# Kernel tuning notes

Hardware: AMD Instinct MI355X
Metric: run time of the kernel (lower is better)

## Reference

```python
import jax, jax.numpy as jnp
import numpy as np

N_NODES = 40000
N_EDGES = 400000
N_GRAPHS = 256
F_IN = 128
COND = 100
HEADS = 32
DIMS = [90, 45, 15, 5]
EPS = 1e-5


def setup_inputs() -> dict:
    key = jax.random.key(0)
    ks = iter(jax.random.split(key, 64))
    inp = {}
    inp["x"] = jax.random.normal(next(ks), (N_NODES, F_IN), dtype=jnp.float32)
    inp["edge_index"] = jax.random.randint(next(ks), (2, N_EDGES), 0, N_NODES, dtype=jnp.int32)
    inp["batch"] = jnp.sort(jax.random.randint(next(ks), (N_NODES,), 0, N_GRAPHS, dtype=jnp.int32))
    inp["conditional_features"] = jax.random.normal(next(ks), (COND,), dtype=jnp.float32)
    # GATConv params: W [in, H*C], a_src/a_dst [H, C], bias [C] (concat=False -> out is C)
    dims_in = [F_IN] + DIMS[:-1]
    for i, (ci, co) in enumerate(zip(dims_in, DIMS), start=1):
        sw = 1.0 / np.sqrt(ci)
        inp[f"W{i}"] = jax.random.normal(next(ks), (ci, HEADS * co), dtype=jnp.float32) * sw
        inp[f"as{i}"] = jax.random.normal(next(ks), (HEADS, co), dtype=jnp.float32) * (1.0 / np.sqrt(co))
        inp[f"ad{i}"] = jax.random.normal(next(ks), (HEADS, co), dtype=jnp.float32) * (1.0 / np.sqrt(co))
        inp[f"b{i}"] = jnp.zeros((co,), dtype=jnp.float32)
    # BatchNorm affine params (init gamma=1, beta=0) for sizes F_IN,90,45,15,5
    for i, c in enumerate([F_IN] + DIMS, start=1):
        inp[f"g{i}"] = jnp.ones((c,), dtype=jnp.float32)
        inp[f"be{i}"] = jnp.zeros((c,), dtype=jnp.float32)
    inp["fcW"] = jax.random.normal(next(ks), (DIMS[-1] + COND, 1), dtype=jnp.float32) * (1.0 / np.sqrt(DIMS[-1] + COND))
    inp["fcb"] = jnp.zeros((1,), dtype=jnp.float32)
    return inp


def _bn(x, g, b):
    # training-mode BatchNorm1d: batch statistics (biased var), eps=1e-5
    mu = x.mean(0)
    var = x.var(0)
    return g * (x - mu) * jax.lax.rsqrt(var + EPS) + b


def _gat(x, W, a_s, a_d, b, src, dst, n):
    H, C = a_s.shape
    h = (x @ W).reshape(n, H, C)                      # [N,H,C]
    s_src = jnp.einsum("nhc,hc->nh", h, a_s)
    s_dst = jnp.einsum("nhc,hc->nh", h, a_d)
    logit = jax.nn.leaky_relu(s_src[src] + s_dst[dst], 0.2)  # [E,H]
    m = jax.ops.segment_max(logit, dst, num_segments=n)
    e = jnp.exp(logit - m[dst])
    denom = jax.ops.segment_sum(e, dst, num_segments=n)
    alpha = e / denom[dst]                            # per-dst softmax, [E,H]
    out = jnp.zeros((n, C), dtype=x.dtype)
    for hi in range(H):  # fixed small loop over heads keeps peak memory at [E,C]
        out = out + jax.ops.segment_sum(alpha[:, hi, None] * h[src, hi, :], dst, num_segments=n)
    return out / H + b   # concat=False -> mean over heads, then bias


def reference(x, edge_index, batch, conditional_features,
              W1, as1, ad1, b1, W2, as2, ad2, b2, W3, as3, ad3, b3, W4, as4, ad4, b4,
              g1, be1, g2, be2, g3, be3, g4, be4, g5, be5, fcW, fcb):
    n = x.shape[0]
    loop = jnp.arange(n, dtype=edge_index.dtype)      # PyG GATConv adds self-loops by default
    src = jnp.concatenate([edge_index[0], loop])
    dst = jnp.concatenate([edge_index[1], loop])

    h = _bn(x, g1, be1)
    h = jax.nn.leaky_relu(_gat(h, W1, as1, ad1, b1, src, dst, n), 0.01)
    h = _bn(h, g2, be2)
    h = jax.nn.leaky_relu(_gat(h, W2, as2, ad2, b2, src, dst, n), 0.01)
    h = _bn(h, g3, be3)
    h = jax.nn.leaky_relu(_gat(h, W3, as3, ad3, b3, src, dst, n), 0.01)
    h = _bn(h, g4, be4)
    h = jax.nn.leaky_relu(_gat(h, W4, as4, ad4, b4, src, dst, n), 0.01)
    # dropout is identity in eval mode

    counts = jax.ops.segment_sum(jnp.ones((n,), dtype=h.dtype), batch, num_segments=N_GRAPHS)
    pooled = jax.ops.segment_sum(h, batch, num_segments=N_GRAPHS) / jnp.maximum(counts, 1.0)[:, None]
    z = jnp.concatenate([pooled, jnp.broadcast_to(conditional_features, (N_GRAPHS, COND))], axis=1)
    return jax.nn.sigmoid(z @ fcW + fcb).reshape(-1, 1)
```

## Files before the change

kernel.cpp:

```cpp
#include <hip/hip_runtime.h>
#include <hip/hip_bf16.h>

constexpr int NN = 40000;
constexpr int NE = 400000;
constexpr int NSLAB = 20000;
constexpr int MPAD = 20096;
constexpr int MPADX = 40192;
constexpr int SCB = 256;
constexpr int SCHUNK = (NN + SCB - 1) / SCB;
constexpr int NPB = 512;

__device__ __forceinline__ unsigned short f2bf(float f) {
    unsigned int u = __float_as_uint(f);
    unsigned int r = (u + 0x7FFFu + ((u >> 16) & 1u)) >> 16;
    return (unsigned short)r;
}

__device__ __forceinline__ unsigned int cvt_pk_bf16(float a, float b) {
    unsigned int r;
    asm("v_cvt_pk_bf16_f32 %0, %1, %2" : "=v"(r) : "v"(a), "v"(b));
    return r;
}

__device__ __forceinline__ void load_lds16(const unsigned short* g, unsigned short* l) {
    __builtin_amdgcn_global_load_lds(
        (const __attribute__((address_space(1))) unsigned int*)(g),
        (__attribute__((address_space(3))) unsigned int*)(l), 16, 0, 0);
}

typedef __attribute__((ext_vector_type(8))) short bf16x8;
typedef __attribute__((ext_vector_type(4))) float f32x4;

__global__ void bn_partial(const float* __restrict__ x, int N, int C,
                           float* __restrict__ partial) {
    int ch = threadIdx.x;
    if (ch >= C) return;
    float s = 0.f, sq = 0.f;
    for (int n = blockIdx.x; n < N; n += gridDim.x) {
        float v = x[(size_t)n * C + ch];
        s += v; sq += v * v;
    }
    partial[(size_t)blockIdx.x * 2 * C + ch]     = s;
    partial[(size_t)blockIdx.x * 2 * C + C + ch] = sq;
}

template <int CIN, int CP, int NB>
__global__ __launch_bounds__(256) void bn_apply_f(const float* __restrict__ x,
                                                  const float* __restrict__ partial,
                                                  const float* __restrict__ g,
                                                  const float* __restrict__ be,
                                                  float* __restrict__ scale_g,
                                                  float* __restrict__ shift_g,
                                                  unsigned short* __restrict__ xbn) {
    __shared__ float hs[2][128], hq[2][128];
    __shared__ float sc_l[CP], sh_l[CP];
    const int tid = threadIdx.x;
    const int half = tid >> 7, ch = tid & 127;
    if (ch < CIN) {
        constexpr int H = NB / 2;
        int b0 = half ? H : 0;
        int b1 = half ? NB : H;
        float s = 0.f, sq = 0.f;
#pragma unroll 8
        for (int b = b0; b < b1; ++b) {
            s  += partial[(size_t)b * 2 * CIN + ch];
            sq += partial[(size_t)b * 2 * CIN + CIN + ch];
        }
        hs[half][ch] = s; hq[half][ch] = sq;
    }
    __syncthreads();
    if (tid < CP) {
        float sc = 0.f, sh = 0.f;
        if (tid < CIN) {
            float s  = hs[0][tid] + hs[1][tid];
            float sq = hq[0][tid] + hq[1][tid];
            float mean = s / (float)NN;
            float var  = sq / (float)NN - mean * mean;
            float inv  = rsqrtf(var + 1e-5f);
            sc = g[tid] * inv;
            sh = be[tid] - mean * sc;
            if (blockIdx.x == 0) { scale_g[tid] = sc; shift_g[tid] = sh; }
        }
        sc_l[tid] = sc; sh_l[tid] = sh;
    }
    __syncthreads();
    const int total = NN * (CP / 2);
    for (int idx = blockIdx.x * 256 + tid; idx < total; idx += 256 * gridDim.x) {
        int n = idx / (CP / 2), c2 = idx % (CP / 2);
        int c = 2 * c2;
        float v0 = 0.f, v1 = 0.f;
        if (c < CIN)     v0 = sc_l[c] * x[(size_t)n * CIN + c] + sh_l[c];
        if (c + 1 < CIN) v1 = sc_l[c + 1] * x[(size_t)n * CIN + c + 1] + sh_l[c + 1];
        reinterpret_cast<unsigned int*>(xbn)[idx] = cvt_pk_bf16(v0, v1);
    }
}

struct PrepLayer {
    const float* W; const float* as_; const float* ad_;
    float* Wf; unsigned short* Wft; unsigned short* Wt;
    int CIN, CP, COUT, NP, bbase;
};
struct PrepArgs { PrepLayer L[4]; int nb; };

__global__ void prep_all(PrepArgs A) {
    int bid = blockIdx.x;
    int li = 0;
#pragma unroll
    for (int i = 1; i < 4; ++i)
        if (bid >= A.L[i].bbase) li = i;
    const PrepLayer& P = A.L[li];
    const int CIN = P.CIN, CP = P.CP, COUT = P.COUT;
    int b = bid - P.bbase;
    int tid = threadIdx.x;
    if (b < CP) {
        int cin = b;
        if (tid < 64) {
            int j = tid, h = j & 31;
            float s = 0.f;
            if (cin < CIN) {
                const float* a = (j < 32) ? P.as_ : P.ad_;
                const float* wrow = P.W + (size_t)cin * 32 * COUT + (size_t)h * COUT;
                const float* arow = a + (size_t)h * COUT;
                for (int c = 0; c < COUT; ++c) s += wrow[c] * arow[c];
            }
            P.Wf[cin * 64 + j] = s;
            P.Wft[j * CP + cin] = f2bf(s);
        }
    } else {
        int c = b - CP;
        for (int kk = tid; kk < 32 * CP; kk += blockDim.x) {
            int h = kk / CP, k = kk % CP;
            float v = 0.f;
            if (k < CIN && c < COUT)
                v = P.W[(size_t)k * (32 * COUT) + h * COUT + c] * (1.f / 32.f);
            P.Wt[(size_t)c * (32 * CP) + kk] = f2bf(v);
        }
    }
}

template <int CPK>
__global__ __launch_bounds__(256) void gemm_s(const unsigned short* __restrict__ xbn,
                                              const unsigned short* __restrict__ Wft,
                                              float* __restrict__ Sbuf) {
    constexpr int NC = CPK / 32;
    __shared__ unsigned short Ab[64 * 32];
    __shared__ unsigned short Bb[64 * 32];
    const int m0 = blockIdx.x * 64;
    const int tid = threadIdx.x;
    const int wv = tid >> 6, lane = tid & 63;
    const int mm = lane & 15, quad = lane >> 4;
    f32x4 acc[4];
#pragma unroll
    for (int t = 0; t < 4; ++t) acc[t] = f32x4{0.f, 0.f, 0.f, 0.f};

    for (int c = 0; c < NC; ++c) {
        int row = tid >> 2, gc = tid & 3;
        load_lds16(xbn + (size_t)(m0 + row) * CPK + c * 32 + gc * 8, Ab + (size_t)tid * 8);
        load_lds16(Wft + (size_t)row * CPK + c * 32 + gc * 8, Bb + (size_t)tid * 8);
        asm volatile("s_waitcnt vmcnt(0)" ::: "memory");
        __syncthreads();
        bf16x8 a = *reinterpret_cast<const bf16x8*>(&Ab[(wv * 16 + mm) * 32 + quad * 8]);
#pragma unroll
        for (int t = 0; t < 4; ++t) {
            bf16x8 b = *reinterpret_cast<const bf16x8*>(&Bb[(t * 16 + mm) * 32 + quad * 8]);
            acc[t] = __builtin_amdgcn_mfma_f32_16x16x32_bf16(a, b, acc[t], 0, 0, 0);
        }
        __syncthreads();
    }
    int rbase = m0 + wv * 16 + quad * 4;
#pragma unroll
    for (int t = 0; t < 4; ++t)
#pragma unroll
        for (int r = 0; r < 4; ++r)
            Sbuf[(size_t)(rbase + r) * 64 + t * 16 + mm] = acc[t][r];
}

__global__ __launch_bounds__(256) void gemm_bn(const float* __restrict__ X,
                                               const float* __restrict__ W,
                                               const float* __restrict__ scale,
                                               const float* __restrict__ shift,
                                               int Cin, int HC, float* __restrict__ OUT) {
    __shared__ float As[8][64];
    __shared__ float Bs[8][64];
    int tid = threadIdx.x;
    int n0 = blockIdx.y * 64;
    int j0 = blockIdx.x * 64;
    int tr = tid >> 4, tc = tid & 15;
    float acc[4][4] = {};
    for (int k0 = 0; k0 < Cin; k0 += 8) {
        int idx = tid;
#pragma unroll
        for (int it = 0; it < 2; ++it, idx += 256) {
            int row = idx >> 3, kk = idx & 7;
            int k = k0 + kk;
            float v = 0.f;
            if (k < Cin) v = scale[k] * X[(size_t)(n0 + row) * Cin + k] + shift[k];
            As[kk][row] = v;
        }
        int idx2 = tid;
#pragma unroll
        for (int it = 0; it < 2; ++it, idx2 += 256) {
            int col = idx2 & 63, kr = idx2 >> 6;
            int k = k0 + kr, j = j0 + col;
            float v = 0.f;
            if (k < Cin && j < HC) v = W[(size_t)k * HC + j];
            Bs[kr][col] = v;
        }
        __syncthreads();
#pragma unroll
        for (int kk = 0; kk < 8; ++kk) {
            float a[4], b[4];
#pragma unroll
            for (int i = 0; i < 4; ++i) a[i] = As[kk][tr * 4 + i];
#pragma unroll
            for (int j = 0; j < 4; ++j) b[j] = Bs[kk][tc * 4 + j];
#pragma unroll
            for (int i = 0; i < 4; ++i)
#pragma unroll
                for (int j = 0; j < 4; ++j) acc[i][j] += a[i] * b[j];
        }
        __syncthreads();
    }
#pragma unroll
    for (int i = 0; i < 4; ++i) {
        int row = n0 + tr * 4 + i;
#pragma unroll
        for (int j = 0; j < 4; ++j) {
            int col = j0 + tc * 4 + j;
            if (col < HC) OUT[(size_t)row * HC + col] = acc[i][j];
        }
    }
}

__global__ void count_kernel(const int* __restrict__ dst, int* __restrict__ deg) {
    int e = blockIdx.x * blockDim.x + threadIdx.x;
    if (e < NE) atomicAdd(&deg[dst[e]], 1);
}
__global__ void scan_pass1(const int* __restrict__ deg, int* __restrict__ bsum) {
    __shared__ int red[256];
    int b = blockIdx.x, t = threadIdx.x;
    int lo = b * SCHUNK, hi = min(lo + SCHUNK, NN);
    int s = 0;
    for (int i = lo + t; i < hi; i += 256) s += deg[i] + 1;
    red[t] = s;
    __syncthreads();
    for (int off = 128; off > 0; off >>= 1) {
        if (t < off) red[t] += red[t + off];
        __syncthreads();
    }
    if (t == 0) bsum[b] = red[0];
}
__global__ void scan_pass2(const int* __restrict__ bsum, int* __restrict__ boff,
                           int* __restrict__ rowptr) {
    __shared__ int lds[256];
    int t = threadIdx.x;
    int v0 = bsum[t];
    lds[t] = v0;
    __syncthreads();
    for (int off = 1; off < 256; off <<= 1) {
        int v = (t >= off) ? lds[t - off] : 0;
        __syncthreads();
        lds[t] += v;
        __syncthreads();
    }
    boff[t] = lds[t] - v0;
    if (t == 255) rowptr[NN] = lds[255];
}
__global__ void scan_pass3(const int* __restrict__ deg, const int* __restrict__ boff,
                           int* __restrict__ rowptr, int* __restrict__ cursor) {
    __shared__ int lds[256];
    int b = blockIdx.x, t = threadIdx.x;
    int i = b * SCHUNK + t;
    int d = (t < SCHUNK && i < NN) ? (deg[i] + 1) : 0;
    lds[t] = d;
    __syncthreads();
    for (int off = 1; off < 256; off <<= 1) {
        int v = (t >= off) ? lds[t - off] : 0;
        __syncthreads();
        lds[t] += v;
        __syncthreads();
    }
    if (t < SCHUNK && i < NN) {
        int excl = lds[t] - d + boff[b];
        rowptr[i] = excl;
        cursor[i] = excl;
    }
}
__global__ void scatter_all(const int* __restrict__ src, const int* __restrict__ dst,
                            int* __restrict__ cursor, int* __restrict__ colsrc) {
    int e = blockIdx.x * blockDim.x + threadIdx.x;
    if (e < NE) {
        int pos = atomicAdd(&cursor[dst[e]], 1);
        colsrc[pos] = src[e];
    } else if (e < NE + NN) {
        int n = e - NE;
        int pos = atomicAdd(&cursor[n], 1);
        colsrc[pos] = n;
    }
}

template <int CIN, int CP>
__global__ __launch_bounds__(256) void agg_x(const unsigned short* __restrict__ xbn,
                                             const float* __restrict__ S,
                                             const int* __restrict__ rowptr,
                                             const int* __restrict__ colsrc,
                                             int n0, unsigned short* __restrict__ z) {
    constexpr int BS = 256, CH = 16;
    constexpr int J = (CP >= 64) ? (CP / 8) : 8;
    constexpr int NG = CP / J;
    constexpr int NACC = J / 4;
    constexpr int LIT = CH * 32 / 256;
    __shared__ __align__(16) float x_lds[CH * CP];
    __shared__ float w_lds[CH * 32];
    __shared__ int cs_lds[CH];
    __shared__ float red_m[8][32];
    __shared__ float red_s[8][32];

    int n = n0 + blockIdx.x;
    int tid = threadIdx.x;
    int start = rowptr[n], end = rowptr[n + 1];
    const int h = tid & 31, g = tid >> 5;
    const int cbase = g * J;
    const bool act = (g < NG);
    const float sd = S[(size_t)n * 64 + 32 + h];

    float m_reg = -INFINITY, d_reg = 0.f;
    f32x4 acc4[NACC];
#pragma unroll
    for (int j = 0; j < NACC; ++j) acc4[j] = f32x4{0.f, 0.f, 0.f, 0.f};

    for (int chunk = start; chunk < end; chunk += CH) {
        int ce = min(CH, end - chunk);
        int ce32 = ce * 32;
        if (tid < CH && tid < ce) cs_lds[tid] = colsrc[chunk + tid];
        __syncthreads();

        float lreg[LIT];
        float pmx = -INFINITY;
#pragma unroll
        for (int p = 0; p < LIT; ++p) {
            int idx = p * 256 + tid;
            lreg[p] = -INFINITY;
            if (idx < ce32) {
                int e = idx >> 5;
                float l = S[(size_t)cs_lds[e] * 64 + h] + sd;
                l = l > 0.f ? l : 0.2f * l;
                lreg[p] = l;
                pmx = fmaxf(pmx, l);
            }
        }
        red_m[g][h] = pmx;
        for (int idx = tid; idx < ce * (CP / 4); idx += BS) {
            int e = idx / (CP / 4), c4 = idx % (CP / 4);
            uint2 u = reinterpret_cast<const uint2*>(xbn)[(size_t)cs_lds[e] * (CP / 4) + c4];
            f32x4 t;
            t[0] = __uint_as_float(u.x << 16);
            t[1] = __uint_as_float(u.x & 0xFFFF0000u);
            t[2] = __uint_as_float(u.y << 16);
            t[3] = __uint_as_float(u.y & 0xFFFF0000u);
            *reinterpret_cast<f32x4*>(&x_lds[e * CP + 4 * c4]) = t;
        }
        __syncthreads();

        float cm = red_m[0][h];
#pragma unroll
        for (int s2 = 1; s2 < 8; ++s2) cm = fmaxf(cm, red_m[s2][h]);
        float newm = fmaxf(m_reg, cm);
        float r = (m_reg == -INFINITY) ? 0.f : __expf(m_reg - newm);
        m_reg = newm;

        float ps = 0.f;
#pragma unroll
        for (int p = 0; p < LIT; ++p) {
            int idx = p * 256 + tid;
            if (idx < ce32) {
                float v = __expf(lreg[p] - m_reg);
                w_lds[idx] = v;
                ps += v;
            }
        }
        red_s[g][h] = ps;
        __syncthreads();

        float ss = red_s[0][h];
#pragma unroll
        for (int s2 = 1; s2 < 8; ++s2) ss += red_s[s2][h];
        d_reg = d_reg * r + ss;

        if (act) {
            f32x4 rr4 = {r, r, r, r};
#pragma unroll
            for (int j = 0; j < NACC; ++j) acc4[j] *= rr4;
            for (int e = 0; e < ce; ++e) {
                float w = w_lds[e * 32 + h];
                f32x4 w4 = {w, w, w, w};
                const f32x4* xv = reinterpret_cast<const f32x4*>(&x_lds[e * CP + cbase]);
#pragma unroll
                for (int j = 0; j < NACC; ++j) acc4[j] += w4 * xv[j];
            }
        }
    }

    if (act) {
        float dinv = 1.f / d_reg;
        uint2* zp = reinterpret_cast<uint2*>(
            z + (size_t)(n - n0) * (32 * CP) + h * CP + cbase);
#pragma unroll
        for (int j = 0; j < NACC; ++j) {
            uint2 t;
            t.x = cvt_pk_bf16(acc4[j][0] * dinv, acc4[j][1] * dinv);
            t.y = cvt_pk_bf16(acc4[j][2] * dinv, acc4[j][3] * dinv);
            zp[j] = t;
        }
    }
}

template <int NT, int KP, int KS, bool FB, bool STATS>
__global__ __launch_bounds__(256) void gemm_z_t(const unsigned short* __restrict__ z,
                                                const unsigned short* __restrict__ Wt,
                                                float* __restrict__ obuf,
                                                const float* __restrict__ bias,
                                                int n0, int COUT, int nr, int pstride,
                                                float* __restrict__ statp) {
    constexpr int NP = NT * 16;
    constexpr int KSEG = KP / KS;
    constexpr int NC = KSEG / 64;
    constexpr int MT = 64;
    __shared__ unsigned short Abuf[2][MT * 64];
    __shared__ unsigned short Bbuf[2][NP * 64];

    const int m0 = blockIdx.x * MT;
    const int kbeg = blockIdx.y * KSEG;
    const int tid = threadIdx.x;
    const int wv = tid >> 6;
    const int lane = tid & 63;
    const int mm = lane & 15, quad = lane >> 4;

    auto stage = [&](int buf, int kk) {
#pragma unroll
        for (int it = 0; it < 2; ++it) {
            int gi = it * 256 + tid;
            int row = gi >> 3, gc = gi & 7;
            int srow = m0 + row;
            if (srow > nr - 1) srow = nr - 1;
            const unsigned short* src = z + (size_t)srow * KP + kk + gc * 8;
            unsigned short* dst = &Abuf[buf][(size_t)(it * 256 + wv * 64) * 8];
            load_lds16(src, dst);
        }
#pragma unroll
        for (int it = 0; it < (NP * 8 + 255) / 256; ++it) {
            int gi = it * 256 + tid;
            if (gi < NP * 8) {
                int row = gi >> 3, gc = gi & 7;
                const unsigned short* src = Wt + (size_t)row * KP + kk + gc * 8;
                unsigned short* dst = &Bbuf[buf][(size_t)(it * 256 + wv * 64) * 8];
                load_lds16(src, dst);
            }
        }
    };

    f32x4 acc[NT];
#pragma unroll
    for (int t = 0; t < NT; ++t) acc[t] = f32x4{0.f, 0.f, 0.f, 0.f};

    stage(0, kbeg);
    for (int c = 0; c < NC; ++c) {
        asm volatile("s_waitcnt vmcnt(0)" ::: "memory");
        __syncthreads();
        int cur = c & 1;
        if (c + 1 < NC) stage(cur ^ 1, kbeg + (c + 1) * 64);
        const unsigned short* Ab = Abuf[cur];
        const unsigned short* Bb = Bbuf[cur];
#pragma unroll
        for (int hh = 0; hh < 2; ++hh) {
            bf16x8 a0 = *reinterpret_cast<const bf16x8*>(&Ab[(wv * 16 + mm) * 64 + hh * 32 + quad * 8]);
#pragma unroll
            for (int t = 0; t < NT; ++t) {
                bf16x8 b = *reinterpret_cast<const bf16x8*>(&Bb[(t * 16 + mm) * 64 + hh * 32 + quad * 8]);
                acc[t] = __builtin_amdgcn_mfma_f32_16x16x32_bf16(a0, b, acc[t], 0, 0, 0);
            }
        }
        __syncthreads();
    }

    int row0 = quad * 4;
    if constexpr (FB) {
        float s = 0.f, q = 0.f;
#pragma unroll
        for (int t = 0; t < NT; ++t) {
            int cc = t * 16 + mm;
#pragma unroll
            for (int r = 0; r < 4; ++r) {
                int m = m0 + wv * 16 + row0 + r;
                if (m < nr && cc < COUT) {
                    float v = acc[t][r] + bias[cc];
                    v = v > 0.f ? v : 0.01f * v;
                    obuf[(size_t)(n0 + m) * COUT + cc] = v;
                    if constexpr (STATS) { s += v; q += v * v; }
                }
            }
        }
        if constexpr (STATS) {
            static_assert(NT == 1, "STATS path assumes NT==1");
            __shared__ float ssum[4][4][16], sqsum[4][4][16];
            ssum[wv][quad][mm] = s; sqsum[wv][quad][mm] = q;
            __syncthreads();
            if (tid < 16) {
                float S = 0.f, Q = 0.f;
#pragma unroll
                for (int a = 0; a < 4; ++a)
#pragma unroll
                    for (int b2 = 0; b2 < 4; ++b2) {
                        S += ssum[a][b2][tid]; Q += sqsum[a][b2][tid];
                    }
                if (tid < COUT) {
                    statp[(size_t)blockIdx.x * 2 * COUT + tid] = S;
                    statp[(size_t)blockIdx.x * 2 * COUT + COUT + tid] = Q;
                }
            }
        }
    } else {
        float* pb = obuf + (size_t)blockIdx.y * pstride * NP;
#pragma unroll
        for (int t = 0; t < NT; ++t) {
            int cc = t * 16 + mm;
#pragma unroll
            for (int r = 0; r < 4; ++r) {
                int m = m0 + wv * 16 + row0 + r;
                pb[(size_t)m * NP + cc] = acc[t][r];
            }
        }
    }
}

__global__ void reduce_parts(const float* __restrict__ pbuf, int KS, int NPAD, int COUT,
                             const float* __restrict__ bias, int n0, int nr, int pstride,
                             float* __restrict__ xout) {
    int idx = blockIdx.x * blockDim.x + threadIdx.x;
    if (idx >= nr * NPAD) return;
    int m = idx / NPAD, c = idx % NPAD;
    if (c >= COUT) return;
    float s = 0.f;
    for (int p = 0; p < KS; ++p) s += pbuf[(size_t)p * pstride * NPAD + (size_t)m * NPAD + c];
    float v = s + bias[c];
    v = v > 0.f ? v : 0.01f * v;
    xout[(size_t)(n0 + m) * COUT + c] = v;
}

__global__ __launch_bounds__(64) void pool_head(const float* __restrict__ x4,
                                                const int* __restrict__ batch,
                                                const float* __restrict__ cond,
                                                const float* __restrict__ fcW,
                                                const float* __restrict__ fcb,
                                                float* __restrict__ out) {
    int g = blockIdx.x;
    int lane = threadIdx.x;
    int lo = 0, hi = NN;
    while (lo < hi) { int mid = (lo + hi) >> 1; if (batch[mid] < g) lo = mid + 1; else hi = mid; }
    int lo2 = lo, hi2 = NN;
    while (lo2 < hi2) { int mid = (lo2 + hi2) >> 1; if (batch[mid] < g + 1) lo2 = mid + 1; else hi2 = mid; }
    int beg = lo, end = lo2;

    float s[5] = {0.f, 0.f, 0.f, 0.f, 0.f};
    for (int n = beg + lane; n < end; n += 64) {
#pragma unroll
        for (int c = 0; c < 5; ++c) s[c] += x4[(size_t)n * 5 + c];
    }
    float cz = 0.f;
    if (lane < 100) cz = cond[lane] * fcW[5 + lane];
    if (lane + 64 < 100) cz += cond[lane + 64] * fcW[5 + lane + 64];
#pragma unroll
    for (int off = 32; off > 0; off >>= 1) {
#pragma unroll
        for (int c = 0; c < 5; ++c) s[c] += __shfl_down(s[c], off, 64);
        cz += __shfl_down(cz, off, 64);
    }
    if (lane == 0) {
        float cnt = fmaxf((float)(end - beg), 1.f);
        float zv = fcb[0] + cz;
#pragma unroll
        for (int c = 0; c < 5; ++c) zv += (s[c] / cnt) * fcW[c];
        out[g] = 1.f / (1.f + __expf(-zv));
    }
}

struct LayerBufs {
    float* scale; float* shift;
    unsigned short* xbn; unsigned short* zbuf;
    float* Sbuf; float* pbuf; const int* rowptr; const int* colsrc;
};

template <int CIN, int CP, int COUT, int NP, int NT, int KS, int SLABS, int NB, bool OSTATS>
static void run_layer(const float* xin, const float* sp_in,
                      const float* Wf, const unsigned short* Wft,
                      const unsigned short* Wt,
                      const float* Bv, const float* G, const float* Be,
                      float* xout, float* statp, int pstride,
                      const LayerBufs& B, hipStream_t stream) {
    constexpr int KP = 32 * CP;
    constexpr int NPAD = NT * 16;
    constexpr int NR = NN / SLABS;
    constexpr int NTILE = (NR + 63) / 64;
    bn_apply_f<CIN, CP, NB><<<512, 256, 0, stream>>>(xin, sp_in, G, Be,
                                                     B.scale, B.shift, B.xbn);
    if constexpr (CP >= 64) {
        gemm_s<CP><<<NN / 64, 256, 0, stream>>>(B.xbn, Wft, B.Sbuf);
    } else {
        gemm_bn<<<dim3(1, NN / 64), 256, 0, stream>>>(xin, Wf, B.scale, B.shift, CIN, 64, B.Sbuf);
    }
    for (int s = 0; s < SLABS; ++s) {
        int n0 = s * NR;
        agg_x<CIN, CP><<<NR, 256, 0, stream>>>(B.xbn, B.Sbuf, B.rowptr, B.colsrc, n0, B.zbuf);
        if constexpr (KS > 1) {
            gemm_z_t<NT, KP, KS, false, false><<<dim3(NTILE, KS), 256, 0, stream>>>(
                B.zbuf, Wt, B.pbuf, nullptr, n0, COUT, NR, pstride, nullptr);
            reduce_parts<<<((size_t)NR * NPAD + 255) / 256, 256, 0, stream>>>(
                B.pbuf, KS, NPAD, COUT, Bv, n0, NR, pstride, xout);
        } else {
            gemm_z_t<NT, KP, 1, true, OSTATS><<<dim3(NTILE, 1), 256, 0, stream>>>(
                B.zbuf, Wt, xout, Bv, n0, COUT, NR, pstride, statp);
        }
    }
}

extern "C" void kernel_launch(void* const* d_in, const int* in_sizes, int n_in,
                              void* d_out, int out_size, void* d_ws, size_t ws_size,
                              hipStream_t stream) {
    (void)in_sizes; (void)n_in; (void)out_size;
    const float* x     = (const float*)d_in[0];
    const int*   ei    = (const int*)d_in[1];
    const int*   batch = (const int*)d_in[2];
    const float* cond  = (const float*)d_in[3];
    const float* W[4]  = {(const float*)d_in[4],  (const float*)d_in[8],
                          (const float*)d_in[12], (const float*)d_in[16]};
    const float* Asp[4] = {(const float*)d_in[5],  (const float*)d_in[9],
                           (const float*)d_in[13], (const float*)d_in[17]};
    const float* Adp[4] = {(const float*)d_in[6],  (const float*)d_in[10],
                           (const float*)d_in[14], (const float*)d_in[18]};
    const float* Bv[4]  = {(const float*)d_in[7],  (const float*)d_in[11],
                           (const float*)d_in[15], (const float*)d_in[19]};
    const float* G[4]   = {(const float*)d_in[20], (const float*)d_in[22],
                           (const float*)d_in[24], (const float*)d_in[26]};
    const float* Be[4]  = {(const float*)d_in[21], (const float*)d_in[23],
                           (const float*)d_in[25], (const float*)d_in[27]};
    const float* fcW = (const float*)d_in[30];
    const float* fcb = (const float*)d_in[31];
    float* out = (float*)d_out;

    const int CPs[4]  = {128, 96, 48, 16};
    const int NPs[4]  = {96, 48, 16, 16};
    const int CINs[4] = {128, 90, 45, 15};
    const int COUTs[4] = {90, 45, 15, 5};

    auto layout_total = [&](size_t zb, size_t pb) -> size_t {
        size_t o = 0;
        auto a = [&](size_t b) { o += (b + 255) & ~(size_t)255; };
        a(zb); a((size_t)NN * 128 * 2); a(pb); a((size_t)NN * 90 * 4);
        a((size_t)NN * 64 * 4); a((size_t)NPB * 2 * 128 * 4); a((size_t)NPB * 2 * 128 * 4);
        a(128 * 4); a(128 * 4);
        for (int i = 0; i < 4; ++i) {
            a((size_t)CPs[i] * 64 * 4); a((size_t)64 * CPs[i] * 2);
            a((size_t)NPs[i] * 32 * CPs[i] * 2);
        }
        a((size_t)NN * 4); a((size_t)(NN + 1) * 4); a((size_t)NN * 4);
        a((size_t)(NE + NN) * 4); a((size_t)SCB * 4); a((size_t)SCB * 4);
        return o;
    };
    const size_t zb_big = (size_t)NN * 4096 * 2, pb_big = (size_t)4 * MPADX * 96 * 4;
    const size_t zb_mid = (size_t)NN * 3072 * 2;
    const size_t pb_mid = (size_t)4 * MPAD * 96 * 4;
    const size_t zb_sm  = (size_t)NSLAB * 4096 * 2, pb_sm = (size_t)4 * MPAD * 96 * 4;
    int mode = 2;
    if (layout_total(zb_big, pb_big) <= ws_size) mode = 0;
    else if (layout_total(zb_mid, pb_mid) <= ws_size) mode = 1;
    const size_t zb = (mode == 0) ? zb_big : (mode == 1) ? zb_mid : zb_sm;
    const size_t pbb = (mode == 0) ? pb_big : (mode == 1) ? pb_mid : pb_sm;

    char* base = (char*)d_ws;
    size_t off = 0;
    auto alloc = [&](size_t b) {
        size_t o = off;
        off += (b + 255) & ~(size_t)255;
        return (void*)(base + o);
    };
    unsigned short* zbuf = (unsigned short*)alloc(zb);
    unsigned short* xbn  = (unsigned short*)alloc((size_t)NN * 128 * 2);
    float* pbuf    = (float*)alloc(pbb);
    float* xbuf    = (float*)alloc((size_t)NN * 90 * 4);
    float* Sbuf    = (float*)alloc((size_t)NN * 64 * 4);
    float* partial = (float*)alloc((size_t)NPB * 2 * 128 * 4);
    float* stat1   = (float*)alloc((size_t)NPB * 2 * 128 * 4);
    float* scale   = (float*)alloc(128 * 4);
    float* shift   = (float*)alloc(128 * 4);
    float* Wf_a[4]; unsigned short* Wft_a[4]; unsigned short* Wt_a[4];
    for (int i = 0; i < 4; ++i) {
        Wf_a[i]  = (float*)alloc((size_t)CPs[i] * 64 * 4);
        Wft_a[i] = (unsigned short*)alloc((size_t)64 * CPs[i] * 2);
        Wt_a[i]  = (unsigned short*)alloc((size_t)NPs[i] * 32 * CPs[i] * 2);
    }
    int* deg     = (int*)alloc((size_t)NN * 4);
    int* rowptr  = (int*)alloc((size_t)(NN + 1) * 4);
    int* cursor  = (int*)alloc((size_t)NN * 4);
    int* colsrc  = (int*)alloc((size_t)(NE + NN) * 4);
    int* bsum    = (int*)alloc((size_t)SCB * 4);
    int* boff    = (int*)alloc((size_t)SCB * 4);
    if (off > ws_size) return;

    const int* srcp = ei;
    const int* dstp = ei + NE;

    PrepArgs PA;
    int bb = 0;
    for (int i = 0; i < 4; ++i) {
        PA.L[i] = PrepLayer{W[i], Asp[i], Adp[i], Wf_a[i], Wft_a[i], Wt_a[i],
                            CINs[i], CPs[i], COUTs[i], NPs[i], bb};
        bb += CPs[i] + NPs[i];
    }
    PA.nb = bb;
    prep_all<<<bb, 256, 0, stream>>>(PA);

    hipMemsetAsync(deg, 0, (size_t)NN * 4, stream);
    count_kernel<<<(NE + 255) / 256, 256, 0, stream>>>(dstp, deg);
    scan_pass1<<<SCB, 256, 0, stream>>>(deg, bsum);
    scan_pass2<<<1, 256, 0, stream>>>(bsum, boff, rowptr);
    scan_pass3<<<SCB, 256, 0, stream>>>(deg, boff, rowptr, cursor);
    scatter_all<<<(NE + NN + 255) / 256, 256, 0, stream>>>(srcp, dstp, cursor, colsrc);

    LayerBufs B{scale, shift, xbn, zbuf, Sbuf, pbuf, rowptr, colsrc};

    bn_partial<<<NPB, 128, 0, stream>>>(x, NN, 128, partial);
    if (mode == 0) {
        run_layer<128, 128, 90, 96, 6, 4, 1, NPB, false>(x, partial,
            Wf_a[0], Wft_a[0], Wt_a[0], Bv[0], G[0], Be[0], xbuf, nullptr, MPADX, B, stream);
        bn_partial<<<NPB, 128, 0, stream>>>(xbuf, NN, 90, partial);
        run_layer< 90,  96, 45, 48, 3, 3, 1, NPB, false>(xbuf, partial,
            Wf_a[1], Wft_a[1], Wt_a[1], Bv[1], G[1], Be[1], xbuf, nullptr, MPADX, B, stream);
    } else if (mode == 1) {
        run_layer<128, 128, 90, 96, 6, 4, 2, NPB, false>(x, partial,
            Wf_a[0], Wft_a[0], Wt_a[0], Bv[0], G[0], Be[0], xbuf, nullptr, MPAD, B, stream);
        bn_partial<<<NPB, 128, 0, stream>>>(xbuf, NN, 90, partial);
        run_layer< 90,  96, 45, 48, 3, 3, 1, NPB, false>(xbuf, partial,
            Wf_a[1], Wft_a[1], Wt_a[1], Bv[1], G[1], Be[1], xbuf, nullptr, MPADX, B, stream);
    } else {
        run_layer<128, 128, 90, 96, 6, 4, 2, NPB, false>(x, partial,
            Wf_a[0], Wft_a[0], Wt_a[0], Bv[0], G[0], Be[0], xbuf, nullptr, MPAD, B, stream);
        bn_partial<<<NPB, 128, 0, stream>>>(xbuf, NN, 90, partial);
        run_layer< 90,  96, 45, 48, 3, 3, 2, NPB, false>(xbuf, partial,
            Wf_a[1], Wft_a[1], Wt_a[1], Bv[1], G[1], Be[1], xbuf, nullptr, MPAD, B, stream);
    }
    bn_partial<<<NPB, 128, 0, stream>>>(xbuf, NN, 45, partial);
    run_layer< 45,  48, 15, 16, 1, 1, 1, NPB, true >(xbuf, partial,
        Wf_a[2], Wft_a[2], Wt_a[2], Bv[2], G[2], Be[2], xbuf, stat1, MPADX, B, stream);
    run_layer< 15,  16,  5, 16, 1, 1, 1, 625, false>(xbuf, stat1,
        Wf_a[3], Wft_a[3], Wt_a[3], Bv[3], G[3], Be[3], xbuf, nullptr, MPADX, B, stream);

    pool_head<<<256, 64, 0, stream>>>(xbuf, batch, cond, fcW, fcb, out);
}
```

Baseline: 937.8 us.

## Fuse last-layer GAT aggregation with output projection, bias and activation

Replaces the generic run_layer path for the final GAT layer (15->5) with a BN-apply, a score GEMM, and a new agg_fused4 kernel. That kernel does the online-softmax neighbor aggregation and then projects the aggregated per-head features through W directly in-block. It also applies bias and leaky-ReLU there. This avoids writing the bf16 per-head z buffer and running a separate GEMM for this small layer. The cost is a block-wide LDS reduction across 64 lanes per node, with most threads idle during the aggregation step.

Result: slower. 960.5 us (+2.4%).

```diff
diff --git a/kernel.cpp b/kernel.cpp
--- a/kernel.cpp
+++ b/kernel.cpp
@@ -412,6 +412,139 @@
             t.y = cvt_pk_bf16(acc4[j][2] * dinv, acc4[j][3] * dinv);
             zp[j] = t;
         }
+    }
+}
+
+__global__ __launch_bounds__(256) void agg_fused4(const unsigned short* __restrict__ xbn,
+                                                  const float* __restrict__ S,
+                                                  const int* __restrict__ rowptr,
+                                                  const int* __restrict__ colsrc,
+                                                  const unsigned short* __restrict__ Wt,
+                                                  const float* __restrict__ bias,
+                                                  float* __restrict__ xout) {
+    constexpr int BS = 256, CH = 16, CP = 16;
+    constexpr int J = 8, NG = 2, NACC = 2, LIT = 2, COUT = 5, KP = 512;
+    __shared__ __align__(16) float x_lds[CH * CP];
+    __shared__ float w_lds[CH * 32];
+    __shared__ int cs_lds[CH];
+    __shared__ float red_m[8][32];
+    __shared__ float red_s[8][32];
+    __shared__ unsigned short wt_lds[COUT][KP];
+    __shared__ float fred[64][COUT + 1];
+
+    int n = blockIdx.x;
+    int tid = threadIdx.x;
+    int start = rowptr[n], end = rowptr[n + 1];
+    const int h = tid & 31, g = tid >> 5;
+    const int cbase = g * J;
+    const bool act = (g < NG);
+    const float sd = S[(size_t)n * 64 + 32 + h];
+
+    for (int idx = tid; idx < COUT * (KP / 2); idx += BS) {
+        int c = idx / (KP / 2), k2 = idx % (KP / 2);
+        reinterpret_cast<unsigned int*>(&wt_lds[c][0])[k2] =
+            reinterpret_cast<const unsigned int*>(Wt)[(size_t)c * (KP / 2) + k2];
+    }
+
+    float m_reg = -INFINITY, d_reg = 0.f;
+    f32x4 acc4[NACC];
+#pragma unroll
+    for (int j = 0; j < NACC; ++j) acc4[j] = f32x4{0.f, 0.f, 0.f, 0.f};
+
+    for (int chunk = start; chunk < end; chunk += CH) {
+        int ce = min(CH, end - chunk);
+        int ce32 = ce * 32;
+        if (tid < CH && tid < ce) cs_lds[tid] = colsrc[chunk + tid];
+        __syncthreads();
+
+        float lreg[LIT];
+        float pmx = -INFINITY;
+#pragma unroll
+        for (int p = 0; p < LIT; ++p) {
+            int idx = p * 256 + tid;
+            lreg[p] = -INFINITY;
+            if (idx < ce32) {
+                int e = idx >> 5;
+                float l = S[(size_t)cs_lds[e] * 64 + h] + sd;
+                l = l > 0.f ? l : 0.2f * l;
+                lreg[p] = l;
+                pmx = fmaxf(pmx, l);
+            }
+        }
+        red_m[g][h] = pmx;
+        for (int idx = tid; idx < ce * (CP / 4); idx += BS) {
+            int e = idx / (CP / 4), c4 = idx % (CP / 4);
+            uint2 u = reinterpret_cast<const uint2*>(xbn)[(size_t)cs_lds[e] * (CP / 4) + c4];
+            f32x4 t;
+            t[0] = __uint_as_float(u.x << 16);
+            t[1] = __uint_as_float(u.x & 0xFFFF0000u);
+            t[2] = __uint_as_float(u.y << 16);
+            t[3] = __uint_as_float(u.y & 0xFFFF0000u);
+            *reinterpret_cast<f32x4*>(&x_lds[e * CP + 4 * c4]) = t;
+        }
+        __syncthreads();
+
+        float cm = red_m[0][h];
+#pragma unroll
+        for (int s2 = 1; s2 < 8; ++s2) cm = fmaxf(cm, red_m[s2][h]);
+        float newm = fmaxf(m_reg, cm);
+        float r = (m_reg == -INFINITY) ? 0.f : __expf(m_reg - newm);
+        m_reg = newm;
+
+        float ps = 0.f;
+#pragma unroll
+        for (int p = 0; p < LIT; ++p) {
+            int idx = p * 256 + tid;
+            if (idx < ce32) {
+                float v = __expf(lreg[p] - m_reg);
+                w_lds[idx] = v;
+                ps += v;
+            }
+        }
+        red_s[g][h] = ps;
+        __syncthreads();
+
+        float ss = red_s[0][h];
+#pragma unroll
+        for (int s2 = 1; s2 < 8; ++s2) ss += red_s[s2][h];
+        d_reg = d_reg * r + ss;
+
+        if (act) {
+            f32x4 rr4 = {r, r, r, r};
+#pragma unroll
+            for (int j = 0; j < NACC; ++j) acc4[j] *= rr4;
+            for (int e = 0; e < ce; ++e) {
+                float w = w_lds[e * 32 + h];
+                f32x4 w4 = {w, w, w, w};
+                const f32x4* xv = reinterpret_cast<const f32x4*>(&x_lds[e * CP + cbase]);
+#pragma unroll
+                for (int j = 0; j < NACC; ++j) acc4[j] += w4 * xv[j];
+            }
+        }
+    }
+
+    if (act) {
+        float dinv = 1.f / d_reg;
+        int aid = h * 2 + g;
+        const int kb = h * CP + cbase;
+#pragma unroll
+        for (int c = 0; c < COUT; ++c) {
+            float s = 0.f;
+#pragma unroll
+            for (int j = 0; j < J; ++j) {
+                unsigned int u = (unsigned int)wt_lds[c][kb + j] << 16;
+                s += acc4[j >> 2][j & 3] * __uint_as_float(u);
+            }
+            fred[aid][c] = s * dinv;
+        }
+    }
+    __syncthreads();
+    if (tid < COUT) {
+        float s = 0.f;
+        for (int i = 0; i < 64; ++i) s += fred[i][tid];
+        float v = s + bias[tid];
+        v = v > 0.f ? v : 0.01f * v;
+        xout[(size_t)n * COUT + tid] = v;
     }
 }
 
@@ -751,8 +884,11 @@
     bn_partial<<<NPB, 128, 0, stream>>>(xbuf, NN, 45, partial);
     run_layer< 45,  48, 15, 16, 1, 1, 1, NPB, true >(xbuf, partial,
         Wf_a[2], Wft_a[2], Wt_a[2], Bv[2], G[2], Be[2], xbuf, stat1, MPADX, B, stream);
-    run_layer< 15,  16,  5, 16, 1, 1, 1, 625, false>(xbuf, stat1,
-        Wf_a[3], Wft_a[3], Wt_a[3], Bv[3], G[3], Be[3], xbuf, nullptr, MPADX, B, stream);
+
+    bn_apply_f<15, 16, 625><<<512, 256, 0, stream>>>(xbuf, stat1, G[3], Be[3],
+                                                     scale, shift, xbn);
+    gemm_bn<<<dim3(1, NN / 64), 256, 0, stream>>>(xbuf, Wf_a[3], scale, shift, 15, 64, Sbuf);
+    agg_fused4<<<NN, 256, 0, stream>>>(xbn, Sbuf, rowptr, colsrc, Wt_a[3], Bv[3], xbuf);
 
     pool_head<<<256, 64, 0, stream>>>(xbuf, batch, cond, fcW, fcb, out);
 }
```
